# Optimization experiments

Hardware: AMD Instinct MI355X
Metric: run time of the kernel (lower is better)

## Reference

```python
import jax, jax.numpy as jnp
import numpy as np

EPSILON = 0.5
B, N0, N1, N_DIM = 128, 128, 128, 32


def setup_inputs() -> dict:
    key = jax.random.key(0)
    ks = jax.random.split(key, 7)
    X = jax.random.normal(ks[0], (B, N_DIM), dtype=jnp.float32)
    t = jax.random.uniform(ks[1], (1,), dtype=jnp.float32, minval=0.05, maxval=0.95)
    Mu0 = jax.random.normal(ks[2], (N0, N_DIM), dtype=jnp.float32)
    Mu1 = jax.random.normal(ks[3], (N1, N_DIM), dtype=jnp.float32)
    # positive diagonal variances
    S0 = jax.random.uniform(ks[4], (N0, N_DIM), dtype=jnp.float32) + 0.5
    S1 = jax.random.uniform(ks[5], (N1, N_DIM), dtype=jnp.float32) + 0.5
    # nonnegative coupling that sums to 1 (stand-in for the EMD plan)
    Lam = jax.random.uniform(ks[6], (N0, N1), dtype=jnp.float32)
    Lam = Lam / jnp.sum(Lam)
    return {"X": X, "t": t, "Mu0": Mu0, "Mu1": Mu1, "S0": S0, "S1": S1, "Lam": Lam}


def reference(X, t, Mu0, Mu1, S0, S1, Lam):
    """GMMflow.calc_u: Gaussian-mixture weighted drift u(X, t)."""
    eps = EPSILON
    t = t.reshape(())  # scalar time
    S0b = S0[:, None, :]   # [N0, 1, n]
    S1b = S1[None, :, :]   # [1, N1, n]
    Ds = jnp.sqrt(4.0 * S0b * S1b + eps ** 4)          # [N0, N1, n]
    Cs = 0.5 * (Ds - eps ** 2)
    Sigma = ((1 - t) ** 2) * S0b + (t ** 2) * S1b + 2 * t * (1 - t) * Cs + (eps ** 2) * t * (1 - t)
    Pt = t * S1b + (1 - t) * Cs
    Qt = (1 - t) * S0b + t * Cs
    St = Pt - Qt - (eps ** 2) * t
    Mut = (1 - t) * Mu0[:, None, :] + t * Mu1[None, :, :]   # [N0, N1, n]
    v = Mu1[None, :, :] - Mu0[:, None, :]                   # [N0, N1, n]
    K = St / Sigma                                          # [N0, N1, n]

    D = X[:, None, None, :] - Mut[None]                     # [B, N0, N1, n]
    U = K[None] * D + v[None]                               # [B, N0, N1, n]
    # Independent-Normal log_prob with the +n/2*log(2*pi) offset cancelled
    logw = jnp.sum(-0.5 * D * D / Sigma[None] - 0.5 * jnp.log(Sigma)[None], axis=-1)  # [B, N0, N1]
    W = jnp.exp(jnp.clip(logw, -50.0, 50.0)) * Lam[None]    # [B, N0, N1]

    num = jnp.einsum('bijn,bij->bn', U, W)                  # weighted drift sum
    den = jnp.sum(W, axis=(1, 2))                           # [B]
    return num / den[:, None]
```

## Files before the change

### kernel.cpp

```cpp
#include <hip/hip_runtime.h>
#include <math.h>

#define BB 128
#define ND 32
#define NIJ 16384
#define EPS2 0.25f
#define EPS4 0.0625f

#define TIJ 64
#define NBLK (NIJ / TIJ)
#define NTHR 1024
#define ROWF 132

#define XS_OFF  8448
#define CC_OFF  13056
#define LAM_OFF 13120
#define LDS_FL  13184
#define STG_ROW 36

#define PART_STRIDE 4224
#define DEN_OFF_P 4096

__global__ __launch_bounds__(NTHR, 4) void gmm_fused(
    const float* __restrict__ Xg,
    const float* __restrict__ tptr,
    const float* __restrict__ Mu0, const float* __restrict__ Mu1,
    const float* __restrict__ S0,  const float* __restrict__ S1,
    const float* __restrict__ Lam,
    float* __restrict__ part)
{
    __shared__ __align__(16) float lds[LDS_FL];

    const int tid  = threadIdx.x;
    const int blk  = blockIdx.x;
    const int ij0g = blk * TIJ;
    const float t   = tptr[0];
    const float omt = 1.0f - t;

    {
        const int r  = tid >> 3;
        const int c4 = (tid & 7) * 4;
        *(float4*)&lds[XS_OFF + r * STG_ROW + c4] =
            *(const float4*)&Xg[tid * 4];
    }

#pragma unroll
    for (int k = 0; k < (TIJ * ND) / NTHR; ++k) {
        const int idx = tid + k * NTHR;
        const int ijl = idx >> 5;
        const int n   = idx & 31;
        const int ij  = ij0g + ijl;
        const int i   = ij >> 7;
        const int j   = ij & 127;
        const float s0  = S0[i * ND + n];
        const float s1  = S1[j * ND + n];
        const float mu0 = Mu0[i * ND + n];
        const float mu1 = Mu1[j * ND + n];
        const float Ds  = sqrtf(4.0f * s0 * s1 + EPS4);
        const float Cs  = 0.5f * (Ds - EPS2);
        const float Sigma = omt * omt * s0 + t * t * s1
                          + 2.0f * t * omt * Cs + EPS2 * t * omt;
        const float St  = (t * s1 + omt * Cs) - (omt * s0 + t * Cs) - EPS2 * t;
        const float Mut = omt * mu0 + t * mu1;
        const float v   = mu1 - mu0;
        const float invS = 1.0f / Sigma;
        const float Kf  = St * invS;
        const float cA  = -0.5f * invS;
        const float cB  = Mut * invS;
        lds[ijl * ROWF + n]      = cA;
        lds[ijl * ROWF + 32 + n] = cB;
        lds[ijl * ROWF + 64 + n] = Kf;
        lds[ijl * ROWF + 96 + n] = v - Kf * Mut;
        float cc = cA * Mut * Mut - 0.5f * __logf(Sigma);
        cc += __shfl_xor(cc, 1);
        cc += __shfl_xor(cc, 2);
        cc += __shfl_xor(cc, 4);
        cc += __shfl_xor(cc, 8);
        cc += __shfl_xor(cc, 16);
        if (n == 0) lds[CC_OFF + ijl] = cc;
    }
    if (tid < TIJ) lds[LAM_OFF + tid] = Lam[ij0g + tid];

    __syncthreads();

    const int gij = tid & 7;
    const int nq  = (tid >> 3) & 3;
    const int bl  = tid >> 5;
    const int n0  = nq * 8;

    float x[4][8];
#pragma unroll
    for (int rb = 0; rb < 4; ++rb) {
        const float4 v4 = *(const float4*)&lds[XS_OFF + (bl + 32 * rb) * STG_ROW + n0];
        const float4 w4 = *(const float4*)&lds[XS_OFF + (bl + 32 * rb) * STG_ROW + n0 + 4];
        x[rb][0] = v4.x; x[rb][1] = v4.y; x[rb][2] = v4.z; x[rb][3] = v4.w;
        x[rb][4] = w4.x; x[rb][5] = w4.y; x[rb][6] = w4.z; x[rb][7] = w4.w;
    }

    float num[4][8];
#pragma unroll
    for (int rb = 0; rb < 4; ++rb)
#pragma unroll
        for (int n = 0; n < 8; ++n) num[rb][n] = 0.0f;
    float den[4] = {0.0f, 0.0f, 0.0f, 0.0f};

#pragma unroll
    for (int it = 0; it < TIJ / 8; ++it) {
        const int ijl = gij + (it << 3);
        const float* __restrict__ row = &lds[ijl * ROWF + n0];
        const float4 a0 = *(const float4*)&row[0];
        const float4 a1 = *(const float4*)&row[4];
        const float4 b0 = *(const float4*)&row[32];
        const float4 b1 = *(const float4*)&row[36];

        float la[4], lb[4];
#pragma unroll
        for (int rb = 0; rb < 4; ++rb) {
            float u = fmaf(fmaf(a0.x, x[rb][0], b0.x), x[rb][0], 0.0f);
            float v = fmaf(fmaf(a0.y, x[rb][1], b0.y), x[rb][1], 0.0f);
            u = fmaf(fmaf(a0.z, x[rb][2], b0.z), x[rb][2], u);
            v = fmaf(fmaf(a0.w, x[rb][3], b0.w), x[rb][3], v);
            u = fmaf(fmaf(a1.x, x[rb][4], b1.x), x[rb][4], u);
            v = fmaf(fmaf(a1.y, x[rb][5], b1.y), x[rb][5], v);
            u = fmaf(fmaf(a1.z, x[rb][6], b1.z), x[rb][6], u);
            v = fmaf(fmaf(a1.w, x[rb][7], b1.w), x[rb][7], v);
            la[rb] = u; lb[rb] = v;
        }

        const float4 k0 = *(const float4*)&row[64];
        const float4 k1 = *(const float4*)&row[68];
        const float4 v0 = *(const float4*)&row[96];
        const float4 v1 = *(const float4*)&row[100];
        const float cc0 = lds[CC_OFF + ijl];
        const float lam = lds[LAM_OFF + ijl];

        float w[4];
#pragma unroll
        for (int rb = 0; rb < 4; ++rb) {
            float lw = la[rb] + lb[rb];
            lw += __shfl_xor(lw, 8);
            lw += __shfl_xor(lw, 16);
            lw = fminf(fmaxf(lw + cc0, -50.0f), 50.0f);
            w[rb] = __expf(lw) * lam;
            den[rb] += w[rb];
        }

#pragma unroll
        for (int rb = 0; rb < 4; ++rb) {
            num[rb][0] = fmaf(w[rb], fmaf(k0.x, x[rb][0], v0.x), num[rb][0]);
            num[rb][1] = fmaf(w[rb], fmaf(k0.y, x[rb][1], v0.y), num[rb][1]);
            num[rb][2] = fmaf(w[rb], fmaf(k0.z, x[rb][2], v0.z), num[rb][2]);
            num[rb][3] = fmaf(w[rb], fmaf(k0.w, x[rb][3], v0.w), num[rb][3]);
            num[rb][4] = fmaf(w[rb], fmaf(k1.x, x[rb][4], v1.x), num[rb][4]);
            num[rb][5] = fmaf(w[rb], fmaf(k1.y, x[rb][5], v1.y), num[rb][5]);
            num[rb][6] = fmaf(w[rb], fmaf(k1.z, x[rb][6], v1.z), num[rb][6]);
            num[rb][7] = fmaf(w[rb], fmaf(k1.w, x[rb][7], v1.w), num[rb][7]);
        }
    }

#pragma unroll
    for (int rb = 0; rb < 4; ++rb) {
#pragma unroll
        for (int c = 0; c < 4; ++c) {
            const float s = (gij & 4) ? num[rb][c] : num[rb][c + 4];
            const float r = __shfl_xor(s, 4);
            num[rb][c] = ((gij & 4) ? num[rb][c + 4] : num[rb][c]) + r;
        }
#pragma unroll
        for (int c = 0; c < 2; ++c) {
            const float s = (gij & 2) ? num[rb][c] : num[rb][c + 2];
            const float r = __shfl_xor(s, 2);
            num[rb][c] = ((gij & 2) ? num[rb][c + 2] : num[rb][c]) + r;
        }
        {
            const float s = (gij & 1) ? num[rb][0] : num[rb][1];
            const float r = __shfl_xor(s, 1);
            num[rb][0] = ((gij & 1) ? num[rb][1] : num[rb][0]) + r;
        }
        den[rb] += __shfl_xor(den[rb], 1);
        den[rb] += __shfl_xor(den[rb], 2);
        den[rb] += __shfl_xor(den[rb], 4);
    }

    float* __restrict__ dstg = part + (size_t)blk * PART_STRIDE;
    const int col = (tid & 31);
#pragma unroll
    for (int rb = 0; rb < 4; ++rb) {
        dstg[(bl + 32 * rb) * 32 + col] = num[rb][0];
    }
    if (col == 0) {
#pragma unroll
        for (int rb = 0; rb < 4; ++rb) {
            dstg[DEN_OFF_P + bl + 32 * rb] = den[rb];
        }
    }
}

__global__ __launch_bounds__(256) void gmm_reduce(
    const float* __restrict__ part,
    float* __restrict__ out)
{
    const int blk = blockIdx.x;
    const int b   = blk >> 1;
    const int nh  = blk & 1;
    const int tid = threadIdx.x;
    const int n16 = tid & 15;
    const int sg  = tid >> 4;
    const int n   = nh * 16 + n16;

    float num = 0.0f, den = 0.0f;
#pragma unroll
    for (int g = 0; g < 16; ++g) {
        const int s = sg + g * 16;
        const size_t base = (size_t)s * PART_STRIDE;
        num += part[base + b * 32 + n];
        den += part[base + DEN_OFF_P + b];
    }

    __shared__ float red[16][18];
    red[sg][n16] = num;
    if (n16 == 0) red[sg][16] = den;
    __syncthreads();

    if (tid < 16) {
        float ns = 0.0f, ds = 0.0f;
#pragma unroll
        for (int k = 0; k < 16; ++k) {
            ns += red[k][tid];
            ds += red[k][16];
        }
        out[b * 32 + nh * 16 + tid] = ns / ds;
    }
}

extern "C" void kernel_launch(void* const* d_in, const int* in_sizes, int n_in,
                              void* d_out, int out_size, void* d_ws, size_t ws_size,
                              hipStream_t stream)
{
    const float* X   = (const float*)d_in[0];
    const float* t   = (const float*)d_in[1];
    const float* Mu0 = (const float*)d_in[2];
    const float* Mu1 = (const float*)d_in[3];
    const float* S0  = (const float*)d_in[4];
    const float* S1  = (const float*)d_in[5];
    const float* Lam = (const float*)d_in[6];
    float* out  = (float*)d_out;
    float* part = (float*)d_ws;

    gmm_fused<<<NBLK, NTHR, 0, stream>>>(X, t, Mu0, Mu1, S0, S1, Lam, part);
    gmm_reduce<<<2 * BB, 256, 0, stream>>>(part, out);
}
```

Baseline: 82.04 us.

## Split batch rows across two blocks per ij tile and vectorize reduction

The fused kernel now launches twice as many blocks with half as many threads. Each block handles 64 of the 128 batch rows for a 64-entry ij tile, which cuts the LDS footprint and loosens per-thread register pressure. The cost is that each block repeats the coefficient precompute for its tile, so that work is done twice overall. The reduction kernel is rewritten to use one block per batch row with float4 loads over the 512 partials.

```diff
diff --git a/kernel.cpp b/kernel.cpp
--- a/kernel.cpp
+++ b/kernel.cpp
@@ -8,18 +8,18 @@
 #define EPS4 0.0625f
 
 #define TIJ 64
-#define NBLK (NIJ / TIJ)
-#define NTHR 1024
+#define NBLK 512
+#define NTHR 512
 #define ROWF 132
 
 #define XS_OFF  8448
-#define CC_OFF  13056
-#define LAM_OFF 13120
-#define LDS_FL  13184
+#define CC_OFF  10752
+#define LAM_OFF 10816
+#define LDS_FL  10880
 #define STG_ROW 36
 
-#define PART_STRIDE 4224
-#define DEN_OFF_P 4096
+#define PART_STRIDE 2112
+#define DEN_OFF_P 2048
 
 __global__ __launch_bounds__(NTHR, 4) void gmm_fused(
     const float* __restrict__ Xg,
@@ -33,15 +33,17 @@
 
     const int tid  = threadIdx.x;
     const int blk  = blockIdx.x;
-    const int ij0g = blk * TIJ;
+    const int ijc  = blk >> 1;
+    const int half = blk & 1;
+    const int ij0g = ijc * TIJ;
+    const int b0   = half * 64;
     const float t   = tptr[0];
     const float omt = 1.0f - t;
 
     {
-        const int r  = tid >> 3;
-        const int c4 = (tid & 7) * 4;
-        *(float4*)&lds[XS_OFF + r * STG_ROW + c4] =
-            *(const float4*)&Xg[tid * 4];
+        const int idx = tid * 4;
+        *(float4*)&lds[XS_OFF + (idx >> 5) * STG_ROW + (idx & 31)] =
+            *(const float4*)&Xg[b0 * ND + idx];
     }
 
 #pragma unroll
@@ -91,8 +93,8 @@
     float x[4][8];
 #pragma unroll
     for (int rb = 0; rb < 4; ++rb) {
-        const float4 v4 = *(const float4*)&lds[XS_OFF + (bl + 32 * rb) * STG_ROW + n0];
-        const float4 w4 = *(const float4*)&lds[XS_OFF + (bl + 32 * rb) * STG_ROW + n0 + 4];
+        const float4 v4 = *(const float4*)&lds[XS_OFF + (bl + 16 * rb) * STG_ROW + n0];
+        const float4 w4 = *(const float4*)&lds[XS_OFF + (bl + 16 * rb) * STG_ROW + n0 + 4];
         x[rb][0] = v4.x; x[rb][1] = v4.y; x[rb][2] = v4.z; x[rb][3] = v4.w;
         x[rb][4] = w4.x; x[rb][5] = w4.y; x[rb][6] = w4.z; x[rb][7] = w4.w;
     }
@@ -110,20 +112,20 @@
         const float* __restrict__ row = &lds[ijl * ROWF + n0];
         const float4 a0 = *(const float4*)&row[0];
         const float4 a1 = *(const float4*)&row[4];
-        const float4 b0 = *(const float4*)&row[32];
-        const float4 b1 = *(const float4*)&row[36];
+        const float4 b0q = *(const float4*)&row[32];
+        const float4 b1q = *(const float4*)&row[36];
 
         float la[4], lb[4];
 #pragma unroll
         for (int rb = 0; rb < 4; ++rb) {
-            float u = fmaf(fmaf(a0.x, x[rb][0], b0.x), x[rb][0], 0.0f);
-            float v = fmaf(fmaf(a0.y, x[rb][1], b0.y), x[rb][1], 0.0f);
-            u = fmaf(fmaf(a0.z, x[rb][2], b0.z), x[rb][2], u);
-            v = fmaf(fmaf(a0.w, x[rb][3], b0.w), x[rb][3], v);
-            u = fmaf(fmaf(a1.x, x[rb][4], b1.x), x[rb][4], u);
-            v = fmaf(fmaf(a1.y, x[rb][5], b1.y), x[rb][5], v);
-            u = fmaf(fmaf(a1.z, x[rb][6], b1.z), x[rb][6], u);
-            v = fmaf(fmaf(a1.w, x[rb][7], b1.w), x[rb][7], v);
+            float u = fmaf(fmaf(a0.x, x[rb][0], b0q.x), x[rb][0], 0.0f);
+            float v = fmaf(fmaf(a0.y, x[rb][1], b0q.y), x[rb][1], 0.0f);
+            u = fmaf(fmaf(a0.z, x[rb][2], b0q.z), x[rb][2], u);
+            v = fmaf(fmaf(a0.w, x[rb][3], b0q.w), x[rb][3], v);
+            u = fmaf(fmaf(a1.x, x[rb][4], b1q.x), x[rb][4], u);
+            v = fmaf(fmaf(a1.y, x[rb][5], b1q.y), x[rb][5], v);
+            u = fmaf(fmaf(a1.z, x[rb][6], b1q.z), x[rb][6], u);
+            v = fmaf(fmaf(a1.w, x[rb][7], b1q.w), x[rb][7], v);
             la[rb] = u; lb[rb] = v;
         }
 
@@ -186,12 +188,12 @@
     const int col = (tid & 31);
 #pragma unroll
     for (int rb = 0; rb < 4; ++rb) {
-        dstg[(bl + 32 * rb) * 32 + col] = num[rb][0];
+        dstg[(bl + 16 * rb) * 32 + col] = num[rb][0];
     }
     if (col == 0) {
 #pragma unroll
         for (int rb = 0; rb < 4; ++rb) {
-            dstg[DEN_OFF_P + bl + 32 * rb] = den[rb];
+            dstg[DEN_OFF_P + bl + 16 * rb] = den[rb];
         }
     }
 }
@@ -200,36 +202,37 @@
     const float* __restrict__ part,
     float* __restrict__ out)
 {
-    const int blk = blockIdx.x;
-    const int b   = blk >> 1;
-    const int nh  = blk & 1;
-    const int tid = threadIdx.x;
-    const int n16 = tid & 15;
-    const int sg  = tid >> 4;
-    const int n   = nh * 16 + n16;
-
-    float num = 0.0f, den = 0.0f;
-#pragma unroll
-    for (int g = 0; g < 16; ++g) {
-        const int s = sg + g * 16;
-        const size_t base = (size_t)s * PART_STRIDE;
-        num += part[base + b * 32 + n];
-        den += part[base + DEN_OFF_P + b];
-    }
-
-    __shared__ float red[16][18];
-    red[sg][n16] = num;
-    if (n16 == 0) red[sg][16] = den;
+    const int b    = blockIdx.x;
+    const int half = b >> 6;
+    const int lb   = b & 63;
+    const int tid  = threadIdx.x;
+    const int c4   = tid & 7;
+    const int sg   = tid >> 3;
+
+    float4 acc = make_float4(0.0f, 0.0f, 0.0f, 0.0f);
+    float accd = 0.0f;
+#pragma unroll
+    for (int g = 0; g < 8; ++g) {
+        const int ijc = sg + g * 32;
+        const size_t base = (size_t)(ijc * 2 + half) * PART_STRIDE;
+        const float4 v = *(const float4*)&part[base + lb * 32 + c4 * 4];
+        acc.x += v.x; acc.y += v.y; acc.z += v.z; acc.w += v.w;
+        accd += part[base + DEN_OFF_P + lb];
+    }
+
+    __shared__ float red[32][36];
+    *(float4*)&red[sg][c4 * 4] = acc;
+    if (c4 == 0) red[sg][32] = accd;
     __syncthreads();
 
-    if (tid < 16) {
+    if (tid < 32) {
         float ns = 0.0f, ds = 0.0f;
 #pragma unroll
-        for (int k = 0; k < 16; ++k) {
+        for (int k = 0; k < 32; ++k) {
             ns += red[k][tid];
-            ds += red[k][16];
-        }
-        out[b * 32 + nh * 16 + tid] = ns / ds;
+            ds += red[k][32];
+        }
+        out[b * 32 + tid] = ns / ds;
     }
 }
 
@@ -248,5 +251,5 @@
     float* part = (float*)d_ws;
 
     gmm_fused<<<NBLK, NTHR, 0, stream>>>(X, t, Mu0, Mu1, S0, S1, Lam, part);
-    gmm_reduce<<<2 * BB, 256, 0, stream>>>(part, out);
+    gmm_reduce<<<BB, 256, 0, stream>>>(part, out);
 }
```

Measured after the change: 82.52 us. No clear change (+0.6%).
